# Performance work log

Hardware: AMD Instinct MI355X
Metric: run time of the kernel (lower is better)

Reference implementation:

```python
import jax, jax.numpy as jnp
import numpy as np

B, T, D = 16, 2048, 512
DB, K, TOPK, WIN = 128, 7, 16, 64
GATE_CAP = 0.5
STRAND_CAP = 0.5
_PHI = 1.618033988749895
_PSI = -0.6180339887498949


def _ln(x, w, b):
    mu = jnp.mean(x, -1, keepdims=True)
    var = jnp.var(x, -1, keepdims=True)
    return (x - mu) * jax.lax.rsqrt(var + 1e-5) * w + b


def setup_inputs() -> dict:
    key = jax.random.key(0)
    ks = jax.random.split(key, 20)
    def nrm(i, shape, scale=1.0):
        return jax.random.normal(ks[i], shape, dtype=jnp.float32) * jnp.float32(scale)
    return {
        'X_write': nrm(0, (B, T, D)),
        'X_read': nrm(1, (B, T, D)),
        'slots': nrm(2, (B, K, DB)),
        'W0': nrm(3, (D, D), D ** -0.5),
        'ln_write_w': jnp.ones((D,), jnp.float32),
        'ln_write_b': jnp.zeros((D,), jnp.float32),
        'W_V': nrm(4, (D, DB), D ** -0.5),
        'W_K_slot': nrm(5, (DB, DB), DB ** -0.5),
        'slot_key_bias': nrm(6, (K, DB), 2.0),
        'W_gate_w': nrm(7, (2 * DB, DB), (2 * DB) ** -0.5),
        'W_gate_b': jnp.full((DB,), -2.0, jnp.float32),
        'ln_strand_w': jnp.ones((DB,), jnp.float32),
        'ln_strand_b': jnp.zeros((DB,), jnp.float32),
        'Ws_Q': nrm(8, (DB, DB), DB ** -0.5),
        'Ws_K': nrm(9, (DB, DB), DB ** -0.5),
        'Ws_V': nrm(10, (DB, DB), DB ** -0.5),
        'lambda_strand': nrm(11, (DB,), 0.5),
        'W_Q_read': nrm(12, (D, DB), D ** -0.5),
        'W_K_read': nrm(13, (DB, DB), DB ** -0.5),
        'W_V_read': nrm(14, (DB, D), DB ** -0.5),
        'render_coeffs': nrm(15, (K, 3, D), 0.2),
        'slot_temps': jnp.ones((K,), jnp.float32),
    }


def _forward(X_write, X_read, slots, W0, ln_write_w, ln_write_b, W_V, W_K_slot,
             slot_key_bias, W_gate_w, W_gate_b, ln_strand_w, ln_strand_b,
             Ws_Q, Ws_K, Ws_V, lambda_strand, W_Q_read, W_K_read, W_V_read,
             render_coeffs, slot_temps):
    scale = jnp.float32(DB ** -0.5)
    W0_sg = jax.lax.stop_gradient(W0)
    X_n = _ln(X_write, ln_write_w, ln_write_b)

    # ---- windowed salience + topk pair selection (no-grad in original) ----
    X_nsg = jax.lax.stop_gradient(X_n)
    X_W0 = X_nsg @ W0_sg.T                      # [B,T,D]
    NEG = jnp.float32(-1e30)
    sal = []
    for o in range(1, WIN + 1):                 # offset j = i - o, fixed small loop
        s = jnp.sum(X_nsg[:, o:, :] * X_W0[:, :-o, :], axis=-1)  # [B, T-o]
        sal.append(jnp.pad(s, ((0, 0), (o, 0)), constant_values=NEG))
    sal = jnp.stack(sal, axis=-1).reshape(B, T * WIN)
    _, flat_idx = jax.lax.top_k(sal, TOPK)      # [B, TOPK]
    i_idx = flat_idx // WIN
    j_idx = i_idx - (flat_idx % WIN + 1)

    # ---- gather pairs, salience-weighted relation vector ----
    x_newer = jnp.take_along_axis(X_n, i_idx[:, :, None], axis=1)   # [B,TOPK,D]
    x_older = jnp.take_along_axis(X_n, j_idx[:, :, None], axis=1)
    pair_sal = jnp.sum(x_newer * (x_older @ W0_sg.T), axis=-1)      # [B,TOPK]
    alpha = jax.nn.softmax(pair_sal, axis=-1)
    rel = (x_newer - x_older) @ W_V                                 # [B,TOPK,DB]
    R_t = jnp.einsum('bk,bkd->bd', alpha, rel)                      # [B,DB]

    # ---- gated slot write ----
    slot_keys = slots @ W_K_slot + slot_key_bias                    # [B,K,DB]
    compat = jnp.einsum('bkd,bd->bk', slot_keys, R_t) * scale * jax.nn.softplus(slot_temps)
    sw = jax.nn.softmax(compat, axis=-1)
    weighted_R = sw[:, :, None] * R_t[:, None, :]                   # [B,K,DB]
    g = jax.nn.sigmoid(jnp.concatenate([slots, weighted_R], -1) @ W_gate_w + W_gate_b)
    slots_upd = (1.0 - g) * slots + g * weighted_R

    # ---- K x K strand mixer ----
    Bn = _ln(slots_upd, ln_strand_w, ln_strand_b)
    sa = jax.nn.softmax(jnp.einsum('bqd,bkd->bqk', Bn @ Ws_Q, Bn @ Ws_K) * scale, axis=-1)
    ctx = sa @ (Bn @ Ws_V)
    slots_next = slots_upd + ctx * jnp.clip(jnp.tanh(lambda_strand), -STRAND_CAP, STRAND_CAP)

    # ---- aux losses ----
    L_persist = jnp.mean((slots_next - slots) ** 2)
    nrm = jnp.maximum(jnp.linalg.norm(slots_next, axis=-1, keepdims=True), 1e-12)
    Bnorm = slots_next / nrm
    cos = jnp.einsum('bkd,bjd->bkj', Bnorm, Bnorm)
    off = ~jnp.eye(K, dtype=bool)
    L_div = jnp.mean((cos ** 2)[:, off])

    # ---- directional gated read attention ----
    q_r = X_read @ W_Q_read                                         # [B,T,DB]
    k_r = slots_next @ W_K_read                                     # [B,K,DB]
    v_r = slots_next @ W_V_read                                     # [B,K,D]
    scores = jnp.einsum('btd,bkd->btk', q_r, k_r) * scale
    q_mean = jnp.mean(X_read, axis=1)                               # [B,D]
    w0q = q_mean @ W0_sg.T
    denom = jnp.float32(_PHI - _PSI)
    phi_q = (w0q - _PSI * q_mean) / denom
    psi_q = (_PHI * q_mean - w0q) / denom
    phi_mag = jnp.linalg.norm(phi_q, axis=-1, keepdims=True)
    psi_mag = jnp.linalg.norm(psi_q, axis=-1, keepdims=True)
    total = phi_mag + psi_mag + 1e-6
    basis = jnp.concatenate([jnp.ones_like(phi_mag), phi_mag / total, psi_mag / total], -1)  # [B,3]
    gate = jnp.clip(jnp.tanh(jnp.einsum('bi,kid->bkd', basis, render_coeffs)), -GATE_CAP, GATE_CAP)
    z = jnp.einsum('btk,bkd->btd', jax.nn.softmax(scores, axis=-1), v_r * gate)
    return z, slots_next, L_persist, L_div


def reference(X_write, X_read, slots, W0, ln_write_w, ln_write_b, W_V, W_K_slot,
              slot_key_bias, W_gate_w, W_gate_b, ln_strand_w, ln_strand_b,
              Ws_Q, Ws_K, Ws_V, lambda_strand, W_Q_read, W_K_read, W_V_read,
              render_coeffs, slot_temps):
    return _forward(X_write, X_read, slots, W0, ln_write_w, ln_write_b, W_V, W_K_slot,
                    slot_key_bias, W_gate_w, W_gate_b, ln_strand_w, ln_strand_b,
                    Ws_Q, Ws_K, Ws_V, lambda_strand, W_Q_read, W_K_read, W_V_read,
                    render_coeffs, slot_temps)
```

## Files before the change

kernel.cpp:

```cpp
#include <hip/hip_runtime.h>
#include <math.h>

#define B_ 16
#define T_ 2048
#define D_ 512
#define DB_ 128
#define K_ 7
#define TOPK_ 16
#define WIN_ 64

static constexpr float SCALE_ = 0.08838834764831845f;
static constexpr float PHI_ = 1.618033988749895f;
static constexpr float PSI_ = -0.6180339887498949f;
static constexpr float INV_DENOM_ = 0.4472135954999579f;
static constexpr float NEGV = -1e30f;
static constexpr float NEGINF = -3.402823466e38f;

typedef __attribute__((ext_vector_type(8))) __bf16 bf16x8;
typedef __attribute__((ext_vector_type(8))) unsigned short u16x8;
typedef __attribute__((ext_vector_type(4))) float f32x4;

__device__ inline float softplusf(float x){
    return fmaxf(x, 0.f) + log1pf(expf(-fabsf(x)));
}
__device__ inline unsigned short f2bf(float x){
    unsigned int u = __float_as_uint(x);
    unsigned int r = (u + 0x7FFFu + ((u >> 16) & 1u)) >> 16;
    return (unsigned short)r;
}
__device__ inline float bf2f(unsigned short h){
    return __uint_as_float(((unsigned int)h) << 16);
}
__device__ inline bf16x8 ld_bf8(const unsigned short* p){
    u16x8 r = *(const u16x8*)p;
    return __builtin_bit_cast(bf16x8, r);
}
__device__ inline unsigned int pkbf(float a, float b){
    unsigned int r;
    asm("v_cvt_pk_bf16_f32 %0, %1, %2" : "=v"(r) : "v"(a), "v"(b));
    return r;
}

__global__ __launch_bounds__(256) void prep_kernel(const float* __restrict__ X,
                                                   const float* __restrict__ w,
                                                   const float* __restrict__ b,
                                                   unsigned short* __restrict__ Xh,
                                                   unsigned short* __restrict__ Xl,
                                                   const float* __restrict__ W0,
                                                   unsigned short* __restrict__ Wh,
                                                   unsigned short* __restrict__ Wl,
                                                   const float* __restrict__ Xr,
                                                   float* __restrict__ qpart)
{
    int bx = blockIdx.x;
    int tid = threadIdx.x;
    if (bx < 32768) {
        int row = bx;
        const float* x = X + (size_t)row * D_;
        float2 v = ((const float2*)x)[tid];
        float s = v.x + v.y, ss = v.x*v.x + v.y*v.y;
        for (int off = 32; off; off >>= 1) { s += __shfl_down(s, off); ss += __shfl_down(ss, off); }
        __shared__ float sh[8];
        int wid = tid >> 6, lane = tid & 63;
        if (lane == 0) { sh[wid] = s; sh[4+wid] = ss; }
        __syncthreads();
        if (tid == 0) {
            float S = sh[0]+sh[1]+sh[2]+sh[3], SS = sh[4]+sh[5]+sh[6]+sh[7];
            float mu = S / (float)D_;
            float var = SS / (float)D_ - mu*mu;
            sh[0] = mu; sh[1] = rsqrtf(var + 1e-5f);
        }
        __syncthreads();
        float mu = sh[0], rs = sh[1];
        float2 wv = ((const float2*)w)[tid];
        float2 bv = ((const float2*)b)[tid];
        float ox = (v.x - mu) * rs * wv.x + bv.x;
        float oy = (v.y - mu) * rs * wv.y + bv.y;
        unsigned short hx = f2bf(ox), hy = f2bf(oy);
        unsigned short lx = f2bf(ox - bf2f(hx)), ly = f2bf(oy - bf2f(hy));
        ((unsigned int*)(Xh + (size_t)row * D_))[tid] = (unsigned int)hx | ((unsigned int)hy << 16);
        ((unsigned int*)(Xl + (size_t)row * D_))[tid] = (unsigned int)lx | ((unsigned int)ly << 16);
    } else if (bx < 33024) {
        int gid = (bx - 32768) * 256 + tid;
        float4 v = ((const float4*)W0)[gid];
        unsigned short h0 = f2bf(v.x), h1 = f2bf(v.y), h2 = f2bf(v.z), h3 = f2bf(v.w);
        ushort4 hv = make_ushort4(h0, h1, h2, h3);
        ushort4 lv = make_ushort4(f2bf(v.x - bf2f(h0)), f2bf(v.y - bf2f(h1)),
                                  f2bf(v.z - bf2f(h2)), f2bf(v.w - bf2f(h3)));
        *(ushort4*)&Wh[(size_t)gid*4] = hv;
        *(ushort4*)&Wl[(size_t)gid*4] = lv;
    } else {
        int idx = bx - 33024;
        int b_ = idx >> 5, c = idx & 31;
        const float* base = Xr + ((size_t)(b_*T_ + c*64)) * D_;
        float s0 = 0.f, s1 = 0.f;
        for (int t = 0; t < 64; t++) {
            s0 += base[(size_t)t*D_ + tid];
            s1 += base[(size_t)t*D_ + tid + 256];
        }
        qpart[((size_t)b_*32 + c)*D_ + tid] = s0;
        qpart[((size_t)b_*32 + c)*D_ + tid + 256] = s1;
    }
}

__global__ __launch_bounds__(256) void gemm_xw0_mfma(const unsigned short* __restrict__ Ah,
                                                     const unsigned short* __restrict__ Al,
                                                     const unsigned short* __restrict__ Wh,
                                                     const unsigned short* __restrict__ Wl,
                                                     unsigned short* __restrict__ Ch,
                                                     unsigned short* __restrict__ Cl)
{
    __shared__ unsigned short sAh[128*40], sAl[128*40], sBh[128*40], sBl[128*40];
    int t0 = blockIdx.x * 128, d0 = blockIdx.y * 128;
    int tid = threadIdx.x;
    int lane = tid & 63, wid = tid >> 6;
    int wr = wid >> 1, wc = wid & 1;
    int fr = lane & 15, kc = (lane >> 4) * 8;

    f32x4 acc[4][4];
    #pragma unroll
    for (int m = 0; m < 4; m++)
        #pragma unroll
        for (int n = 0; n < 4; n++) acc[m][n] = (f32x4){0.f,0.f,0.f,0.f};

    int srow = tid >> 1, skh = (tid & 1) * 16;

    for (int kk = 0; kk < 512; kk += 32) {
        const unsigned short* gAh = Ah + (size_t)(t0 + srow)*512 + kk + skh;
        const unsigned short* gAl = Al + (size_t)(t0 + srow)*512 + kk + skh;
        const unsigned short* gWh = Wh + (size_t)(d0 + srow)*512 + kk + skh;
        const unsigned short* gWl = Wl + (size_t)(d0 + srow)*512 + kk + skh;
        int so = srow*40 + skh;
        *(uint4*)&sAh[so]     = *(const uint4*)(gAh);
        *(uint4*)&sAh[so + 8] = *(const uint4*)(gAh + 8);
        *(uint4*)&sAl[so]     = *(const uint4*)(gAl);
        *(uint4*)&sAl[so + 8] = *(const uint4*)(gAl + 8);
        *(uint4*)&sBh[so]     = *(const uint4*)(gWh);
        *(uint4*)&sBh[so + 8] = *(const uint4*)(gWh + 8);
        *(uint4*)&sBl[so]     = *(const uint4*)(gWl);
        *(uint4*)&sBl[so + 8] = *(const uint4*)(gWl + 8);
        __syncthreads();

        bf16x8 ah[4], al[4], bh[4], bl[4];
        #pragma unroll
        for (int m = 0; m < 4; m++) {
            int r = (wr*64 + m*16 + fr)*40 + kc;
            ah[m] = ld_bf8(&sAh[r]);
            al[m] = ld_bf8(&sAl[r]);
        }
        #pragma unroll
        for (int n = 0; n < 4; n++) {
            int r = (wc*64 + n*16 + fr)*40 + kc;
            bh[n] = ld_bf8(&sBh[r]);
            bl[n] = ld_bf8(&sBl[r]);
        }
        #pragma unroll
        for (int m = 0; m < 4; m++)
            #pragma unroll
            for (int n = 0; n < 4; n++) {
                acc[m][n] = __builtin_amdgcn_mfma_f32_16x16x32_bf16(bh[n], ah[m], acc[m][n], 0, 0, 0);
                acc[m][n] = __builtin_amdgcn_mfma_f32_16x16x32_bf16(bh[n], al[m], acc[m][n], 0, 0, 0);
                acc[m][n] = __builtin_amdgcn_mfma_f32_16x16x32_bf16(bl[n], ah[m], acc[m][n], 0, 0, 0);
            }
        __syncthreads();
    }

    #pragma unroll
    for (int m = 0; m < 4; m++) {
        int t = t0 + wr*64 + m*16 + fr;
        #pragma unroll
        for (int n = 0; n < 4; n++) {
            int dbase = d0 + wc*64 + n*16 + (lane >> 4)*4;
            float a0 = acc[m][n][0], a1 = acc[m][n][1], a2 = acc[m][n][2], a3 = acc[m][n][3];
            unsigned int h01 = pkbf(a0, a1), h23 = pkbf(a2, a3);
            float r0 = a0 - __uint_as_float(h01 << 16);
            float r1 = a1 - __uint_as_float(h01 & 0xFFFF0000u);
            float r2 = a2 - __uint_as_float(h23 << 16);
            float r3 = a3 - __uint_as_float(h23 & 0xFFFF0000u);
            unsigned int l01 = pkbf(r0, r1), l23 = pkbf(r2, r3);
            uint2 hv; hv.x = h01; hv.y = h23;
            uint2 lv; lv.x = l01; lv.y = l23;
            *(uint2*)&Ch[(size_t)t*512 + dbase] = hv;
            *(uint2*)&Cl[(size_t)t*512 + dbase] = lv;
        }
    }
}

__global__ __launch_bounds__(256) void sal_mfma(const unsigned short* __restrict__ Xh,
                                                const unsigned short* __restrict__ Xl,
                                                const unsigned short* __restrict__ Wh,
                                                const unsigned short* __restrict__ Wl,
                                                float* __restrict__ sal)
{
    int b = blockIdx.x, i0 = blockIdx.y * 64;
    __shared__ unsigned short sAh[64*40], sAl[64*40], sBh[128*40], sBl[128*40];
    int tid = threadIdx.x;
    int lane = tid & 63, wc = tid >> 6;
    int fr = lane & 15, kc = (lane >> 4) * 8;

    const unsigned short* XhB = Xh + (size_t)b*T_*D_;
    const unsigned short* XlB = Xl + (size_t)b*T_*D_;
    const unsigned short* WhB = Wh + (size_t)b*T_*D_;
    const unsigned short* WlB = Wl + (size_t)b*T_*D_;

    f32x4 acc[4][2];
    #pragma unroll
    for (int m = 0; m < 4; m++) { acc[m][0] = (f32x4){0.f,0.f,0.f,0.f}; acc[m][1] = (f32x4){0.f,0.f,0.f,0.f}; }

    int arow = tid >> 2, akh = (tid & 3) * 8;
    int brow = tid >> 1, bkh = (tid & 1) * 16;
    int jrow = i0 - 64 + brow;
    const uint4 z4 = make_uint4(0,0,0,0);

    for (int kk = 0; kk < 512; kk += 32) {
        *(uint4*)&sAh[arow*40 + akh] = *(const uint4*)(XhB + (size_t)(i0 + arow)*512 + kk + akh);
        *(uint4*)&sAl[arow*40 + akh] = *(const uint4*)(XlB + (size_t)(i0 + arow)*512 + kk + akh);
        int bo = brow*40 + bkh;
        if (jrow >= 0) {
            const unsigned short* gh = WhB + (size_t)jrow*512 + kk + bkh;
            const unsigned short* gl = WlB + (size_t)jrow*512 + kk + bkh;
            *(uint4*)&sBh[bo]     = *(const uint4*)(gh);
            *(uint4*)&sBh[bo + 8] = *(const uint4*)(gh + 8);
            *(uint4*)&sBl[bo]     = *(const uint4*)(gl);
            *(uint4*)&sBl[bo + 8] = *(const uint4*)(gl + 8);
        } else {
            *(uint4*)&sBh[bo] = z4; *(uint4*)&sBh[bo + 8] = z4;
            *(uint4*)&sBl[bo] = z4; *(uint4*)&sBl[bo + 8] = z4;
        }
        __syncthreads();

        bf16x8 ah[4], al[4], bh[2], bl[2];
        #pragma unroll
        for (int m = 0; m < 4; m++) {
            int r = (m*16 + fr)*40 + kc;
            ah[m] = ld_bf8(&sAh[r]);
            al[m] = ld_bf8(&sAl[r]);
        }
        #pragma unroll
        for (int n = 0; n < 2; n++) {
            int r = (wc*32 + n*16 + fr)*40 + kc;
            bh[n] = ld_bf8(&sBh[r]);
            bl[n] = ld_bf8(&sBl[r]);
        }
        #pragma unroll
        for (int m = 0; m < 4; m++)
            #pragma unroll
            for (int n = 0; n < 2; n++) {
                acc[m][n] = __builtin_amdgcn_mfma_f32_16x16x32_bf16(ah[m], bh[n], acc[m][n], 0, 0, 0);
                acc[m][n] = __builtin_amdgcn_mfma_f32_16x16x32_bf16(ah[m], bl[n], acc[m][n], 0, 0, 0);
                acc[m][n] = __builtin_amdgcn_mfma_f32_16x16x32_bf16(al[m], bh[n], acc[m][n], 0, 0, 0);
            }
        __syncthreads();
    }

    float* salB = sal + (size_t)b*T_*WIN_;
    #pragma unroll
    for (int m = 0; m < 4; m++) {
        #pragma unroll
        for (int n = 0; n < 2; n++) {
            int jl = wc*32 + n*16 + fr;
            #pragma unroll
            for (int r = 0; r < 4; r++) {
                int il = m*16 + (lane >> 4)*4 + r;
                int o = il - jl + 64;
                if (o >= 1 && o <= 64) {
                    int jg = i0 - 64 + jl;
                    salB[(size_t)(i0 + il)*WIN_ + (o - 1)] = (jg >= 0) ? acc[m][n][r] : NEGV;
                }
            }
        }
    }
}

__global__ __launch_bounds__(256) void topk_stage1(const float* __restrict__ sal,
                                                   float* __restrict__ cv, int* __restrict__ ci)
{
    int b = blockIdx.x, c = blockIdx.y;
    const float* s = sal + (size_t)b*(T_*WIN_) + (size_t)c*2048;
    int base = c*2048;
    int tid = threadIdx.x;
    int lane = tid & 63, wvi = tid >> 6;
    float lv[8]; int li[8];
    #pragma unroll
    for (int k = 0; k < 8; k++) { lv[k] = NEGINF; li[k] = 0x7FFFFFFF; }
    #pragma unroll
    for (int r = 0; r < 8; r++) {
        int p = tid + r*256;
        float v = s[p];
        int idx = base + p;
        if (v > lv[7]) {
            int k = 7;
            while (k > 0 && lv[k-1] < v) { lv[k] = lv[k-1]; li[k] = li[k-1]; k--; }
            lv[k] = v; li[k] = idx;
        }
    }
    float* cvo = cv + (((size_t)b*64 + c)*64) + wvi*16;
    int*   cio = ci + (((size_t)b*64 + c)*64) + wvi*16;
    int head = 0;
    for (int r = 0; r < 16; r++) {
        float bv = (head < 8) ? lv[head] : NEGINF;
        int   bi = (head < 8) ? li[head] : 0x7FFFFFFF;
        float wv_ = bv; int wi = bi;
        #pragma unroll
        for (int off = 1; off < 64; off <<= 1) {
            float v2 = __shfl_xor(wv_, off);
            int   i2 = __shfl_xor(wi, off);
            if (v2 > wv_ || (v2 == wv_ && i2 < wi)) { wv_ = v2; wi = i2; }
        }
        if (bv == wv_ && bi == wi) head++;
        if (lane == 0) { cvo[r] = wv_; cio[r] = wi; }
    }
}

__global__ __launch_bounds__(1024) void slot_kernel(
    const unsigned short* __restrict__ Xh, const unsigned short* __restrict__ Xl,
    const float* __restrict__ slots_in,
    const float* __restrict__ cv, const int* __restrict__ ci,
    const float* __restrict__ W_V, const float* __restrict__ W_K_slot, const float* __restrict__ skb,
    const float* __restrict__ Wg, const float* __restrict__ Wgb,
    const float* __restrict__ lnw, const float* __restrict__ lnb,
    const float* __restrict__ WsQ, const float* __restrict__ WsK, const float* __restrict__ WsV,
    const float* __restrict__ lambda_, const float* __restrict__ temps,
    float* __restrict__ snws, float* __restrict__ out_slots,
    float* __restrict__ lpP, float* __restrict__ lpD)
{
    int b = blockIdx.x, tid = threadIdx.x;
    int lane = tid & 63, wvi = tid >> 6;
    __shared__ float alpha[16];
    __shared__ int   tis[16], tjs[16];
    __shared__ float tvv[16]; __shared__ int tii[16];
    __shared__ float scv[256]; __shared__ int sci[256];
    __shared__ float y[D_];
    __shared__ float part[8][DB_];
    __shared__ float pf[1024];
    __shared__ float Rt[DB_];
    __shared__ float sl[K_][DB_];
    __shared__ float upd[K_][DB_];
    __shared__ float Bn[K_][DB_];
    __shared__ float qq[K_][DB_], kk2[K_][DB_], vv[K_][DB_];
    __shared__ float snsh[K_][DB_];
    __shared__ float swv[K_], compat[K_], mu7[K_], rs7[K_], nr7[K_], ldv[K_];
    __shared__ float sa[K_][K_];

    for (int p = tid; p < K_*DB_; p += 1024) sl[p>>7][p&127] = slots_in[(size_t)b*K_*DB_ + p];

    {
        const float* cvb = cv + (size_t)b*4096;
        const int*   cib = ci + (size_t)b*4096;
        float lv[4]; int li[4];
        #pragma unroll
        for (int k = 0; k < 4; k++) { lv[k] = NEGINF; li[k] = 0x7FFFFFFF; }
        #pragma unroll
        for (int r = 0; r < 4; r++) {
            int p = tid + r*1024;
            float v = cvb[p];
            int idx = cib[p];
            if (v > lv[3] || (v == lv[3] && idx < li[3])) {
                int k = 3;
                while (k > 0 && (lv[k-1] < v || (lv[k-1] == v && li[k-1] > idx))) {
                    lv[k] = lv[k-1]; li[k] = li[k-1]; k--;
                }
                lv[k] = v; li[k] = idx;
            }
        }
        int head = 0;
        for (int r = 0; r < 16; r++) {
            float bv = (head < 4) ? lv[head] : NEGINF;
            int   bi = (head < 4) ? li[head] : 0x7FFFFFFF;
            float wv_ = bv; int wi = bi;
            #pragma unroll
            for (int off = 1; off < 64; off <<= 1) {
                float v2 = __shfl_xor(wv_, off);
                int   i2 = __shfl_xor(wi, off);
                if (v2 > wv_ || (v2 == wv_ && i2 < wi)) { wv_ = v2; wi = i2; }
            }
            if (bv == wv_ && bi == wi) head++;
            if (lane == 0) { scv[wvi*16 + r] = wv_; sci[wvi*16 + r] = wi; }
        }
        __syncthreads();
        if (wvi == 0) {
            float mv[4]; int mi[4];
            #pragma unroll
            for (int k = 0; k < 4; k++) { mv[k] = NEGINF; mi[k] = 0x7FFFFFFF; }
            #pragma unroll
            for (int r = 0; r < 4; r++) {
                int p = lane + r*64;
                float v = scv[p]; int idx = sci[p];
                if (v > mv[3] || (v == mv[3] && idx < mi[3])) {
                    int k = 3;
                    while (k > 0 && (mv[k-1] < v || (mv[k-1] == v && mi[k-1] > idx))) {
                        mv[k] = mv[k-1]; mi[k] = mi[k-1]; k--;
                    }
                    mv[k] = v; mi[k] = idx;
                }
            }
            int head2 = 0;
            for (int r = 0; r < 16; r++) {
                float bv = (head2 < 4) ? mv[head2] : NEGINF;
                int   bi = (head2 < 4) ? mi[head2] : 0x7FFFFFFF;
                float wv_ = bv; int wi = bi;
                #pragma unroll
                for (int off = 1; off < 64; off <<= 1) {
                    float v2 = __shfl_xor(wv_, off);
                    int   i2 = __shfl_xor(wi, off);
                    if (v2 > wv_ || (v2 == wv_ && i2 < wi)) { wv_ = v2; wi = i2; }
                }
                if (bv == wv_ && bi == wi) head2++;
                if (lane == 0) { tvv[r] = wv_; tii[r] = wi; }
            }
        }
        __syncthreads();
    }
    if (tid < 16) {
        float v = tvv[tid];
        int flat = tii[tid];
        tis[tid] = flat >> 6;
        tjs[tid] = (flat >> 6) - ((flat & 63) + 1);
        float m = v;
        #pragma unroll
        for (int off = 8; off; off >>= 1) m = fmaxf(m, __shfl_xor(m, off, 16));
        float e = expf(v - m);
        float s = e;
        #pragma unroll
        for (int off = 8; off; off >>= 1) s += __shfl_xor(s, off, 16);
        alpha[tid] = e / s;
    }
    __syncthreads();

    if (tid < D_) {
        float acc = 0.f;
        #pragma unroll
        for (int k = 0; k < 16; k++) {
            int i = tis[k], j = tjs[k];
            float xi = bf2f(Xh[((size_t)b*T_ + i)*D_ + tid]) + bf2f(Xl[((size_t)b*T_ + i)*D_ + tid]);
            float xj = bf2f(Xh[((size_t)b*T_ + j)*D_ + tid]) + bf2f(Xl[((size_t)b*T_ + j)*D_ + tid]);
            acc += alpha[k] * (xi - xj);
        }
        y[tid] = acc;
    }
    __syncthreads();

    {
        int g = tid >> 7, d = tid & 127;
        float acc = 0.f;
        int e0 = g * 64;
        for (int e = e0; e < e0 + 64; e++) acc += y[e] * W_V[(size_t)e*DB_ + d];
        part[g][d] = acc;
    }
    __syncthreads();
    if (tid < DB_) {
        float acc = 0.f;
        #pragma unroll
        for (int g = 0; g < 8; g++) acc += part[g][tid];
        Rt[tid] = acc;
    }
    __syncthreads();

    if (tid < K_*DB_) {
        int k = tid >> 7, d = tid & 127;
        float acc = skb[k*DB_ + d];
        for (int e = 0; e < DB_; e++) acc += sl[k][e] * W_K_slot[(size_t)e*DB_ + d];
        qq[k][d] = acc * Rt[d];
    }
    __syncthreads();
    if (wvi < K_) {
        float acc = qq[wvi][lane] + qq[wvi][lane + 64];
        #pragma unroll
        for (int off = 32; off; off >>= 1) acc += __shfl_xor(acc, off);
        if (lane == 0) compat[wvi] = acc * SCALE_ * softplusf(temps[wvi]);
    }
    __syncthreads();
    if (tid == 0) {
        float m = compat[0];
        for (int k = 1; k < K_; k++) m = fmaxf(m, compat[k]);
        float ssum = 0.f;
        for (int k = 0; k < K_; k++) { float e = expf(compat[k]-m); swv[k] = e; ssum += e; }
        for (int k = 0; k < K_; k++) swv[k] /= ssum;
    }
    __syncthreads();

    if (tid < K_*DB_) {
        int k = tid >> 7, d = tid & 127;
        float swk = swv[k];
        float acc = Wgb[d];
        for (int e = 0; e < DB_; e++) acc += sl[k][e] * Wg[(size_t)e*DB_ + d];
        for (int e = 0; e < DB_; e++) acc += swk * Rt[e] * Wg[(size_t)(DB_+e)*DB_ + d];
        float g = 1.f / (1.f + expf(-acc));
        upd[k][d] = (1.f - g) * sl[k][d] + g * (swk * Rt[d]);
    }
    __syncthreads();

    if (wvi < K_) {
        float v0 = upd[wvi][lane], v1 = upd[wvi][lane + 64];
        float s = v0 + v1, ss = v0*v0 + v1*v1;
        #pragma unroll
        for (int off = 32; off; off >>= 1) { s += __shfl_xor(s, off); ss += __shfl_xor(ss, off); }
        if (lane == 0) {
            float mu = s / (float)DB_;
            mu7[wvi] = mu;
            rs7[wvi] = rsqrtf(ss/(float)DB_ - mu*mu + 1e-5f);
        }
    }
    __syncthreads();
    if (tid < K_*DB_) {
        int k = tid >> 7, d = tid & 127;
        Bn[k][d] = (upd[k][d] - mu7[k]) * rs7[k] * lnw[d] + lnb[d];
    }
    __syncthreads();

    if (tid < K_*DB_) {
        int k = tid >> 7, d = tid & 127;
        float aq = 0.f, ak = 0.f, av = 0.f;
        for (int e = 0; e < DB_; e++) {
            float bn = Bn[k][e];
            aq += bn * WsQ[(size_t)e*DB_ + d];
            ak += bn * WsK[(size_t)e*DB_ + d];
            av += bn * WsV[(size_t)e*DB_ + d];
        }
        qq[k][d] = aq; kk2[k][d] = ak; vv[k][d] = av;
    }
    __syncthreads();

    if (wvi < K_) {
        int j = lane >> 3, s = lane & 7;
        float acc = 0.f;
        if (j < K_) {
            int e0 = s * 16;
            for (int e = e0; e < e0 + 16; e++) acc += qq[wvi][e] * kk2[j][e];
        }
        #pragma unroll
        for (int off = 4; off; off >>= 1) acc += __shfl_xor(acc, off, 8);
        if (s == 0 && j < K_) sa[wvi][j] = acc * SCALE_;
    }
    __syncthreads();
    if (tid < K_) {
        float m = sa[tid][0];
        for (int j = 1; j < K_; j++) m = fmaxf(m, sa[tid][j]);
        float ssum = 0.f;
        for (int j = 0; j < K_; j++) { float e = expf(sa[tid][j]-m); sa[tid][j] = e; ssum += e; }
        for (int j = 0; j < K_; j++) sa[tid][j] /= ssum;
    }
    __syncthreads();

    if (tid < K_*DB_) {
        int k = tid >> 7, d = tid & 127;
        float lam = tanhf(lambda_[d]);
        lam = fminf(fmaxf(lam, -0.5f), 0.5f);
        float c = 0.f;
        #pragma unroll
        for (int j = 0; j < K_; j++) c += sa[k][j] * vv[j][d];
        float sn = upd[k][d] + c * lam;
        snsh[k][d] = sn;
        snws[((size_t)b*K_ + k)*DB_ + d] = sn;
        out_slots[((size_t)b*K_ + k)*DB_ + d] = sn;
    }
    __syncthreads();

    {
        float dsq = 0.f;
        if (tid < K_*DB_) {
            int k = tid >> 7, d = tid & 127;
            float dd = snsh[k][d] - sl[k][d];
            dsq = dd*dd;
        }
        pf[tid] = dsq;
        if (wvi < K_) {
            float v0 = snsh[wvi][lane], v1 = snsh[wvi][lane + 64];
            float ss = v0*v0 + v1*v1;
            #pragma unroll
            for (int off = 32; off; off >>= 1) ss += __shfl_xor(ss, off);
            if (lane == 0) nr7[wvi] = fmaxf(sqrtf(ss), 1e-12f);
        }
        __syncthreads();
        if (wvi == 0) {
            float s = 0.f;
            #pragma unroll
            for (int q = 0; q < 16; q++) s += pf[lane + q*64];
            #pragma unroll
            for (int off = 32; off; off >>= 1) s += __shfl_xor(s, off);
            if (lane == 0) lpP[b] = s;
        }
        if (wvi >= 1 && wvi <= K_) {
            int q = wvi - 1;
            float accq = 0.f;
            for (int j = 0; j < K_; j++) {
                if (j == q) continue;
                float dt = snsh[q][lane]*snsh[j][lane] + snsh[q][lane+64]*snsh[j][lane+64];
                #pragma unroll
                for (int off = 32; off; off >>= 1) dt += __shfl_xor(dt, off);
                float cs = dt / (nr7[q] * nr7[j]);
                accq += cs*cs;
            }
            if (lane == 0) ldv[q] = accq;
        }
        __syncthreads();
        if (tid == 0) {
            float s = 0.f;
            for (int q = 0; q < K_; q++) s += ldv[q];
            lpD[b] = s;
        }
    }
}

__global__ __launch_bounds__(256) void w0q_part_kernel(const float* __restrict__ qpart,
                                                       const float* __restrict__ W0,
                                                       float* __restrict__ w0p)
{
    int b = blockIdx.x, c = blockIdx.y, tid = threadIdx.x;
    __shared__ float qm[D_];
    for (int p = tid; p < D_; p += 256) {
        float s = 0.f;
        for (int cc = 0; cc < 32; cc++) s += qpart[((size_t)b*32 + cc)*D_ + p];
        qm[p] = s * (1.f/2048.f);
    }
    __syncthreads();
    int w = tid >> 6, lane = tid & 63;
    float ph = 0.f, ps = 0.f;
    for (int r = 0; r < 16; r++) {
        int d = c*64 + w*16 + r;
        const float* wr = W0 + (size_t)d*D_;
        float s = 0.f;
        #pragma unroll
        for (int q = 0; q < 8; q++) s += qm[lane + q*64] * wr[lane + q*64];
        #pragma unroll
        for (int off = 32; off; off >>= 1) s += __shfl_xor(s, off);
        float phi = (s - PSI_*qm[d]) * INV_DENOM_;
        float psi = (PHI_*qm[d] - s) * INV_DENOM_;
        ph += phi*phi; ps += psi*psi;
    }
    __shared__ float shp[4], shs[4];
    if (lane == 0) { shp[w] = ph; shs[w] = ps; }
    __syncthreads();
    if (tid == 0) {
        w0p[((size_t)b*8 + c)*2 + 0] = shp[0]+shp[1]+shp[2]+shp[3];
        w0p[((size_t)b*8 + c)*2 + 1] = shs[0]+shs[1]+shs[2]+shs[3];
    }
}

__global__ __launch_bounds__(256) void kqvg_kernel(
    const float* __restrict__ sn, const float* __restrict__ WKr,
    const float* __restrict__ WQr, const float* __restrict__ WVr,
    const float* __restrict__ rc, const float* __restrict__ w0p,
    const float* __restrict__ lpP, const float* __restrict__ lpD,
    float* __restrict__ kq, float* __restrict__ vg, float* __restrict__ loss_out)
{
    int b = blockIdx.x, k = blockIdx.y, tid = threadIdx.x;
    if (b == 0 && k == 0 && tid == 0) {
        float s = 0.f, s2 = 0.f;
        for (int bb = 0; bb < B_; bb++) { s += lpP[bb]; s2 += lpD[bb]; }
        loss_out[0] = s / (float)(B_*K_*DB_);
        loss_out[1] = s2 / (float)(B_*(K_*K_-K_));
    }
    float P = 0.f, Q = 0.f;
    #pragma unroll
    for (int c = 0; c < 8; c++) {
        P += w0p[((size_t)b*8 + c)*2 + 0];
        Q += w0p[((size_t)b*8 + c)*2 + 1];
    }
    float pm = sqrtf(P), qm2 = sqrtf(Q);
    float tot = pm + qm2 + 1e-6f;
    float b1 = pm / tot, b2 = qm2 / tot;

    __shared__ float sl[DB_], kr[DB_];
    if (tid < DB_) sl[tid] = sn[((size_t)b*K_ + k)*DB_ + tid];
    __syncthreads();
    if (tid < DB_) {
        float a = 0.f;
        for (int e = 0; e < DB_; e++) a += sl[e] * WKr[(size_t)e*DB_ + tid];
        kr[tid] = a;
    }
    __syncthreads();
    #pragma unroll
    for (int rep = 0; rep < 2; rep++) {
        int e = tid + rep*256;
        float a = 0.f;
        const float* wq = WQr + (size_t)e*DB_;
        for (int d = 0; d < DB_; d++) a += kr[d] * wq[d];
        kq[((size_t)b*K_ + k)*D_ + e] = a;
    }
    #pragma unroll
    for (int rep = 0; rep < 2; rep++) {
        int dd = tid + rep*256;
        float a = 0.f;
        for (int e = 0; e < DB_; e++) a += sl[e] * WVr[(size_t)e*D_ + dd];
        float gpre = rc[((size_t)k*3 + 0)*D_ + dd] + b1*rc[((size_t)k*3 + 1)*D_ + dd] + b2*rc[((size_t)k*3 + 2)*D_ + dd];
        float g = tanhf(gpre);
        g = fminf(fmaxf(g, -0.5f), 0.5f);
        vg[((size_t)b*K_ + k)*D_ + dd] = a * g;
    }
}

__global__ __launch_bounds__(256) void z_kernel(const float* __restrict__ Xr,
                                                const float* __restrict__ kq,
                                                const float* __restrict__ vg,
                                                float* __restrict__ z)
{
    int b = blockIdx.x;
    int t0 = blockIdx.y * 64;
    __shared__ float kqs[K_][D_];
    __shared__ float vgs[K_][D_];
    int tid = threadIdx.x;
    for (int p = tid; p < K_*D_; p += 256) {
        kqs[p>>9][p&511] = kq[(size_t)b*K_*D_ + p];
        vgs[p>>9][p&511] = vg[(size_t)b*K_*D_ + p];
    }
    __syncthreads();
    int lane = tid & 63, w = tid >> 6;
    for (int it = 0; it < 16; it++) {
        int t = t0 + w*16 + it;
        const float* x = Xr + ((size_t)b*T_ + t)*D_;
        float xr[8];
        float s[K_] = {0,0,0,0,0,0,0};
        #pragma unroll
        for (int r = 0; r < 8; r++) {
            int e = lane + r*64;
            xr[r] = x[e];
            #pragma unroll
            for (int k = 0; k < K_; k++) s[k] += xr[r] * kqs[k][e];
        }
        #pragma unroll
        for (int k = 0; k < K_; k++)
            for (int off = 32; off; off >>= 1) s[k] += __shfl_xor(s[k], off);
        float sc[K_];
        float m = NEGINF;
        #pragma unroll
        for (int k = 0; k < K_; k++) { sc[k] = s[k] * SCALE_; m = fmaxf(m, sc[k]); }
        float p[K_], ssum = 0.f;
        #pragma unroll
        for (int k = 0; k < K_; k++) { p[k] = expf(sc[k] - m); ssum += p[k]; }
        float inv = 1.f / ssum;
        float* zp = z + ((size_t)b*T_ + t)*D_;
        #pragma unroll
        for (int r = 0; r < 8; r++) {
            int e = lane + r*64;
            float a = 0.f;
            #pragma unroll
            for (int k = 0; k < K_; k++) a += p[k] * vgs[k][e];
            zp[e] = a * inv;
        }
    }
}

extern "C" void kernel_launch(void* const* d_in, const int* in_sizes, int n_in,
                              void* d_out, int out_size, void* d_ws, size_t ws_size,
                              hipStream_t stream)
{
    const float* X_write = (const float*)d_in[0];
    const float* X_read  = (const float*)d_in[1];
    const float* slots   = (const float*)d_in[2];
    const float* W0      = (const float*)d_in[3];
    const float* lnw_w   = (const float*)d_in[4];
    const float* lnw_b   = (const float*)d_in[5];
    const float* W_V     = (const float*)d_in[6];
    const float* W_K_slot= (const float*)d_in[7];
    const float* skb     = (const float*)d_in[8];
    const float* Wg      = (const float*)d_in[9];
    const float* Wgb     = (const float*)d_in[10];
    const float* lns_w   = (const float*)d_in[11];
    const float* lns_b   = (const float*)d_in[12];
    const float* WsQ     = (const float*)d_in[13];
    const float* WsK     = (const float*)d_in[14];
    const float* WsV     = (const float*)d_in[15];
    const float* lambda_ = (const float*)d_in[16];
    const float* WQr     = (const float*)d_in[17];
    const float* WKr     = (const float*)d_in[18];
    const float* WVr     = (const float*)d_in[19];
    const float* rc      = (const float*)d_in[20];
    const float* temps   = (const float*)d_in[21];

    const size_t NXD = (size_t)B_*T_*D_;
    unsigned short* Xh  = (unsigned short*)d_ws;
    unsigned short* Xl  = Xh + NXD;
    unsigned short* Ch  = Xl + NXD;
    unsigned short* Cl  = Ch + NXD;
    unsigned short* W0h = Cl + NXD;
    unsigned short* W0l = W0h + (size_t)D_*D_;
    float* fscr  = (float*)(W0l + (size_t)D_*D_);
    float* qpart = fscr;
    float* w0p   = qpart + (size_t)B_*32*D_;
    float* snws  = w0p + 256;
    float* kq    = snws + (size_t)B_*K_*DB_;
    float* vg    = kq + (size_t)B_*K_*D_;
    float* cv    = vg + (size_t)B_*K_*D_;
    int*   ci    = (int*)(cv + (size_t)B_*64*64);
    float* lpP   = (float*)(ci + (size_t)B_*64*64);
    float* lpD   = lpP + 16;

    float* z_out     = (float*)d_out;
    float* slots_out = z_out + NXD;
    float* loss_out  = slots_out + (size_t)B_*K_*DB_;
    float* sal       = z_out;

    prep_kernel<<<dim3(32768 + 256 + 512), dim3(256), 0, stream>>>(
        X_write, lnw_w, lnw_b, Xh, Xl, W0, W0h, W0l, X_read, qpart);
    gemm_xw0_mfma<<<dim3(B_*T_/128, D_/128), dim3(256), 0, stream>>>(Xh, Xl, W0h, W0l, Ch, Cl);
    sal_mfma<<<dim3(B_, T_/64), dim3(256), 0, stream>>>(Xh, Xl, Ch, Cl, sal);
    topk_stage1<<<dim3(B_, 64), dim3(256), 0, stream>>>(sal, cv, ci);
    slot_kernel<<<dim3(B_), dim3(1024), 0, stream>>>(Xh, Xl, slots, cv, ci,
        W_V, W_K_slot, skb, Wg, Wgb, lns_w, lns_b, WsQ, WsK, WsV, lambda_, temps,
        snws, slots_out, lpP, lpD);
    w0q_part_kernel<<<dim3(B_, 8), dim3(256), 0, stream>>>(qpart, W0, w0p);
    kqvg_kernel<<<dim3(B_, K_), dim3(256), 0, stream>>>(snws, WKr, WQr, WVr, rc, w0p,
        lpP, lpD, kq, vg, loss_out);
    z_kernel<<<dim3(B_, T_/64), dim3(256), 0, stream>>>(X_read, kq, vg, z_out);
}
```

Baseline: 312.9 us.

## Use direct global-to-LDS loads with XOR-swizzled LDS and fp32 GEMM output

The X·W0 GEMM now stages tiles through global_load_lds, with each wave loading one of the four operand arrays. The padded LDS rows become unpadded rows with a rotation swizzle, which reduces LDS footprint and avoids bank conflicts. The GEMM epilogue now writes fp32 directly instead of a split bf16 hi/lo pair, and the hi/lo split moves into the salience kernel's B-tile load. This cuts the GEMM's store work and removes register staging, at the cost of the salience kernel reading fp32 and redoing the split for each overlapping window tile.

```diff
diff --git a/kernel.cpp b/kernel.cpp
--- a/kernel.cpp
+++ b/kernel.cpp
@@ -39,6 +39,11 @@
     unsigned int r;
     asm("v_cvt_pk_bf16_f32 %0, %1, %2" : "=v"(r) : "v"(a), "v"(b));
     return r;
+}
+typedef __attribute__((address_space(3))) unsigned int as3_u32;
+typedef const __attribute__((address_space(1))) unsigned int as1_u32c;
+__device__ inline void gload16(const void* g, void* l){
+    __builtin_amdgcn_global_load_lds((as1_u32c*)g, (as3_u32*)l, 16, 0, 0);
 }
 
 __global__ __launch_bounds__(256) void prep_kernel(const float* __restrict__ X,
@@ -107,15 +112,15 @@
                                                      const unsigned short* __restrict__ Al,
                                                      const unsigned short* __restrict__ Wh,
                                                      const unsigned short* __restrict__ Wl,
-                                                     unsigned short* __restrict__ Ch,
-                                                     unsigned short* __restrict__ Cl)
+                                                     float* __restrict__ Cf)
 {
-    __shared__ unsigned short sAh[128*40], sAl[128*40], sBh[128*40], sBl[128*40];
+    __shared__ __align__(16) unsigned short sAh[128*32], sAl[128*32], sBh[128*32], sBl[128*32];
     int t0 = blockIdx.x * 128, d0 = blockIdx.y * 128;
     int tid = threadIdx.x;
     int lane = tid & 63, wid = tid >> 6;
     int wr = wid >> 1, wc = wid & 1;
-    int fr = lane & 15, kc = (lane >> 4) * 8;
+    int fr = lane & 15;
+    int kc2 = ((((lane >> 4) + (fr >> 1)) & 3) * 8);
 
     f32x4 acc[4][4];
     #pragma unroll
@@ -123,44 +128,38 @@
         #pragma unroll
         for (int n = 0; n < 4; n++) acc[m][n] = (f32x4){0.f,0.f,0.f,0.f};
 
-    int srow = tid >> 1, skh = (tid & 1) * 16;
+    const unsigned short* gs = (wid==0) ? Ah : (wid==1) ? Al : (wid==2) ? Wh : Wl;
+    unsigned short* ls = (wid==0) ? sAh : (wid==1) ? sAl : (wid==2) ? sBh : sBl;
+    int rowoff = (wid < 2) ? t0 : d0;
+    int cch = ((lane & 3) - ((lane >> 3) & 3)) & 3;
+    const unsigned short* gbase = gs + (size_t)(rowoff + (lane >> 2))*512 + cch*8;
 
     for (int kk = 0; kk < 512; kk += 32) {
-        const unsigned short* gAh = Ah + (size_t)(t0 + srow)*512 + kk + skh;
-        const unsigned short* gAl = Al + (size_t)(t0 + srow)*512 + kk + skh;
-        const unsigned short* gWh = Wh + (size_t)(d0 + srow)*512 + kk + skh;
-        const unsigned short* gWl = Wl + (size_t)(d0 + srow)*512 + kk + skh;
-        int so = srow*40 + skh;
-        *(uint4*)&sAh[so]     = *(const uint4*)(gAh);
-        *(uint4*)&sAh[so + 8] = *(const uint4*)(gAh + 8);
-        *(uint4*)&sAl[so]     = *(const uint4*)(gAl);
-        *(uint4*)&sAl[so + 8] = *(const uint4*)(gAl + 8);
-        *(uint4*)&sBh[so]     = *(const uint4*)(gWh);
-        *(uint4*)&sBh[so + 8] = *(const uint4*)(gWh + 8);
-        *(uint4*)&sBl[so]     = *(const uint4*)(gWl);
-        *(uint4*)&sBl[so + 8] = *(const uint4*)(gWl + 8);
-        __syncthreads();
-
-        bf16x8 ah[4], al[4], bh[4], bl[4];
+        #pragma unroll
+        for (int i = 0; i < 8; i++)
+            gload16(gbase + (size_t)(16*i)*512 + kk, ls + i*512);
+        __syncthreads();
+
+        bf16x8 ahf[4], alf[4], bhf[4], blf[4];
         #pragma unroll
         for (int m = 0; m < 4; m++) {
-            int r = (wr*64 + m*16 + fr)*40 + kc;
-            ah[m] = ld_bf8(&sAh[r]);
-            al[m] = ld_bf8(&sAl[r]);
+            int r = (wr*64 + m*16 + fr)*32 + kc2;
+            ahf[m] = ld_bf8(&sAh[r]);
+            alf[m] = ld_bf8(&sAl[r]);
         }
         #pragma unroll
         for (int n = 0; n < 4; n++) {
-            int r = (wc*64 + n*16 + fr)*40 + kc;
-            bh[n] = ld_bf8(&sBh[r]);
-            bl[n] = ld_bf8(&sBl[r]);
+            int r = (wc*64 + n*16 + fr)*32 + kc2;
+            bhf[n] = ld_bf8(&sBh[r]);
+            blf[n] = ld_bf8(&sBl[r]);
         }
         #pragma unroll
         for (int m = 0; m < 4; m++)
             #pragma unroll
             for (int n = 0; n < 4; n++) {
-                acc[m][n] = __builtin_amdgcn_mfma_f32_16x16x32_bf16(bh[n], ah[m], acc[m][n], 0, 0, 0);
-                acc[m][n] = __builtin_amdgcn_mfma_f32_16x16x32_bf16(bh[n], al[m], acc[m][n], 0, 0, 0);
-                acc[m][n] = __builtin_amdgcn_mfma_f32_16x16x32_bf16(bl[n], ah[m], acc[m][n], 0, 0, 0);
+                acc[m][n] = __builtin_amdgcn_mfma_f32_16x16x32_bf16(bhf[n], ahf[m], acc[m][n], 0, 0, 0);
+                acc[m][n] = __builtin_amdgcn_mfma_f32_16x16x32_bf16(bhf[n], alf[m], acc[m][n], 0, 0, 0);
+                acc[m][n] = __builtin_amdgcn_mfma_f32_16x16x32_bf16(blf[n], ahf[m], acc[m][n], 0, 0, 0);
             }
         __syncthreads();
     }
@@ -171,84 +170,88 @@
         #pragma unroll
         for (int n = 0; n < 4; n++) {
             int dbase = d0 + wc*64 + n*16 + (lane >> 4)*4;
-            float a0 = acc[m][n][0], a1 = acc[m][n][1], a2 = acc[m][n][2], a3 = acc[m][n][3];
-            unsigned int h01 = pkbf(a0, a1), h23 = pkbf(a2, a3);
-            float r0 = a0 - __uint_as_float(h01 << 16);
-            float r1 = a1 - __uint_as_float(h01 & 0xFFFF0000u);
-            float r2 = a2 - __uint_as_float(h23 << 16);
-            float r3 = a3 - __uint_as_float(h23 & 0xFFFF0000u);
-            unsigned int l01 = pkbf(r0, r1), l23 = pkbf(r2, r3);
-            uint2 hv; hv.x = h01; hv.y = h23;
-            uint2 lv; lv.x = l01; lv.y = l23;
-            *(uint2*)&Ch[(size_t)t*512 + dbase] = hv;
-            *(uint2*)&Cl[(size_t)t*512 + dbase] = lv;
+            *(f32x4*)&Cf[(size_t)t*512 + dbase] = acc[m][n];
         }
     }
 }
 
 __global__ __launch_bounds__(256) void sal_mfma(const unsigned short* __restrict__ Xh,
                                                 const unsigned short* __restrict__ Xl,
-                                                const unsigned short* __restrict__ Wh,
-                                                const unsigned short* __restrict__ Wl,
+                                                const float* __restrict__ Cf,
                                                 float* __restrict__ sal)
 {
     int b = blockIdx.x, i0 = blockIdx.y * 64;
-    __shared__ unsigned short sAh[64*40], sAl[64*40], sBh[128*40], sBl[128*40];
+    __shared__ __align__(16) unsigned short sAh[64*32], sAl[64*32], sBh[128*32], sBl[128*32];
     int tid = threadIdx.x;
-    int lane = tid & 63, wc = tid >> 6;
-    int fr = lane & 15, kc = (lane >> 4) * 8;
+    int lane = tid & 63, wcw = tid >> 6;
+    int fr = lane & 15;
+    int kc2 = ((((lane >> 4) + (fr >> 1)) & 3) * 8);
 
     const unsigned short* XhB = Xh + (size_t)b*T_*D_;
     const unsigned short* XlB = Xl + (size_t)b*T_*D_;
-    const unsigned short* WhB = Wh + (size_t)b*T_*D_;
-    const unsigned short* WlB = Wl + (size_t)b*T_*D_;
+    const float* CfB = Cf + (size_t)b*T_*D_;
 
     f32x4 acc[4][2];
     #pragma unroll
     for (int m = 0; m < 4; m++) { acc[m][0] = (f32x4){0.f,0.f,0.f,0.f}; acc[m][1] = (f32x4){0.f,0.f,0.f,0.f}; }
 
-    int arow = tid >> 2, akh = (tid & 3) * 8;
-    int brow = tid >> 1, bkh = (tid & 1) * 16;
+    int ar = tid >> 2, ac = tid & 3;
+    int aslot = (ac + (ar >> 1)) & 3;
+    int brow = tid >> 1, bhh = tid & 1;
     int jrow = i0 - 64 + brow;
-    const uint4 z4 = make_uint4(0,0,0,0);
 
     for (int kk = 0; kk < 512; kk += 32) {
-        *(uint4*)&sAh[arow*40 + akh] = *(const uint4*)(XhB + (size_t)(i0 + arow)*512 + kk + akh);
-        *(uint4*)&sAl[arow*40 + akh] = *(const uint4*)(XlB + (size_t)(i0 + arow)*512 + kk + akh);
-        int bo = brow*40 + bkh;
-        if (jrow >= 0) {
-            const unsigned short* gh = WhB + (size_t)jrow*512 + kk + bkh;
-            const unsigned short* gl = WlB + (size_t)jrow*512 + kk + bkh;
-            *(uint4*)&sBh[bo]     = *(const uint4*)(gh);
-            *(uint4*)&sBh[bo + 8] = *(const uint4*)(gh + 8);
-            *(uint4*)&sBl[bo]     = *(const uint4*)(gl);
-            *(uint4*)&sBl[bo + 8] = *(const uint4*)(gl + 8);
-        } else {
-            *(uint4*)&sBh[bo] = z4; *(uint4*)&sBh[bo + 8] = z4;
-            *(uint4*)&sBl[bo] = z4; *(uint4*)&sBl[bo + 8] = z4;
-        }
-        __syncthreads();
-
-        bf16x8 ah[4], al[4], bh[2], bl[2];
+        *(uint4*)&sAh[ar*32 + aslot*8] = *(const uint4*)(XhB + (size_t)(i0 + ar)*512 + kk + ac*8);
+        *(uint4*)&sAl[ar*32 + aslot*8] = *(const uint4*)(XlB + (size_t)(i0 + ar)*512 + kk + ac*8);
+        #pragma unroll
+        for (int cc = 0; cc < 2; cc++) {
+            int c = 2*bhh + cc;
+            int slot = (c + (brow >> 1)) & 3;
+            uint4 hv, lv;
+            if (jrow >= 0) {
+                const float* src = CfB + (size_t)jrow*512 + kk + c*8;
+                float4 v0 = *(const float4*)src;
+                float4 v1 = *(const float4*)(src + 4);
+                unsigned int h01 = pkbf(v0.x, v0.y), h23 = pkbf(v0.z, v0.w);
+                unsigned int h45 = pkbf(v1.x, v1.y), h67 = pkbf(v1.z, v1.w);
+                float r0 = v0.x - __uint_as_float(h01 << 16);
+                float r1 = v0.y - __uint_as_float(h01 & 0xFFFF0000u);
+                float r2 = v0.z - __uint_as_float(h23 << 16);
+                float r3 = v0.w - __uint_as_float(h23 & 0xFFFF0000u);
+                float r4 = v1.x - __uint_as_float(h45 << 16);
+                float r5 = v1.y - __uint_as_float(h45 & 0xFFFF0000u);
+                float r6 = v1.z - __uint_as_float(h67 << 16);
+                float r7 = v1.w - __uint_as_float(h67 & 0xFFFF0000u);
+                hv.x = h01; hv.y = h23; hv.z = h45; hv.w = h67;
+                lv.x = pkbf(r0, r1); lv.y = pkbf(r2, r3); lv.z = pkbf(r4, r5); lv.w = pkbf(r6, r7);
+            } else {
+                hv = make_uint4(0,0,0,0); lv = make_uint4(0,0,0,0);
+            }
+            *(uint4*)&sBh[brow*32 + slot*8] = hv;
+            *(uint4*)&sBl[brow*32 + slot*8] = lv;
+        }
+        __syncthreads();
+
+        bf16x8 ahf[4], alf[4], bhf[2], blf[2];
         #pragma unroll
         for (int m = 0; m < 4; m++) {
-            int r = (m*16 + fr)*40 + kc;
-            ah[m] = ld_bf8(&sAh[r]);
-            al[m] = ld_bf8(&sAl[r]);
+            int r = (m*16 + fr)*32 + kc2;
+            ahf[m] = ld_bf8(&sAh[r]);
+            alf[m] = ld_bf8(&sAl[r]);
         }
         #pragma unroll
         for (int n = 0; n < 2; n++) {
-            int r = (wc*32 + n*16 + fr)*40 + kc;
-            bh[n] = ld_bf8(&sBh[r]);
-            bl[n] = ld_bf8(&sBl[r]);
+            int r = (wcw*32 + n*16 + fr)*32 + kc2;
+            bhf[n] = ld_bf8(&sBh[r]);
+            blf[n] = ld_bf8(&sBl[r]);
         }
         #pragma unroll
         for (int m = 0; m < 4; m++)
             #pragma unroll
             for (int n = 0; n < 2; n++) {
-                acc[m][n] = __builtin_amdgcn_mfma_f32_16x16x32_bf16(ah[m], bh[n], acc[m][n], 0, 0, 0);
-                acc[m][n] = __builtin_amdgcn_mfma_f32_16x16x32_bf16(ah[m], bl[n], acc[m][n], 0, 0, 0);
-                acc[m][n] = __builtin_amdgcn_mfma_f32_16x16x32_bf16(al[m], bh[n], acc[m][n], 0, 0, 0);
+                acc[m][n] = __builtin_amdgcn_mfma_f32_16x16x32_bf16(ahf[m], bhf[n], acc[m][n], 0, 0, 0);
+                acc[m][n] = __builtin_amdgcn_mfma_f32_16x16x32_bf16(ahf[m], blf[n], acc[m][n], 0, 0, 0);
+                acc[m][n] = __builtin_amdgcn_mfma_f32_16x16x32_bf16(alf[m], bhf[n], acc[m][n], 0, 0, 0);
             }
         __syncthreads();
     }
@@ -258,7 +261,7 @@
     for (int m = 0; m < 4; m++) {
         #pragma unroll
         for (int n = 0; n < 2; n++) {
-            int jl = wc*32 + n*16 + fr;
+            int jl = wcw*32 + n*16 + fr;
             #pragma unroll
             for (int r = 0; r < 4; r++) {
                 int il = m*16 + (lane >> 4)*4 + r;
@@ -771,9 +774,8 @@
     const size_t NXD = (size_t)B_*T_*D_;
     unsigned short* Xh  = (unsigned short*)d_ws;
     unsigned short* Xl  = Xh + NXD;
-    unsigned short* Ch  = Xl + NXD;
-    unsigned short* Cl  = Ch + NXD;
-    unsigned short* W0h = Cl + NXD;
+    float* Cf           = (float*)(Xl + NXD);
+    unsigned short* W0h = (unsigned short*)(Cf + NXD);
     unsigned short* W0l = W0h + (size_t)D_*D_;
     float* fscr  = (float*)(W0l + (size_t)D_*D_);
     float* qpart = fscr;
@@ -793,8 +795,8 @@
 
     prep_kernel<<<dim3(32768 + 256 + 512), dim3(256), 0, stream>>>(
         X_write, lnw_w, lnw_b, Xh, Xl, W0, W0h, W0l, X_read, qpart);
-    gemm_xw0_mfma<<<dim3(B_*T_/128, D_/128), dim3(256), 0, stream>>>(Xh, Xl, W0h, W0l, Ch, Cl);
-    sal_mfma<<<dim3(B_, T_/64), dim3(256), 0, stream>>>(Xh, Xl, Ch, Cl, sal);
+    gemm_xw0_mfma<<<dim3(B_*T_/128, D_/128), dim3(256), 0, stream>>>(Xh, Xl, W0h, W0l, Cf);
+    sal_mfma<<<dim3(B_, T_/64), dim3(256), 0, stream>>>(Xh, Xl, Cf, sal);
     topk_stage1<<<dim3(B_, 64), dim3(256), 0, stream>>>(sal, cv, ci);
     slot_kernel<<<dim3(B_), dim3(1024), 0, stream>>>(Xh, Xl, slots, cv, ci,
         W_V, W_K_slot, skb, Wg, Wgb, lns_w, lns_b, WsQ, WsK, WsV, lambda_, temps,
```

Result: faster. 304.2 us (-2.8%).
